# Performance work log

Hardware: AMD Instinct MI355X
Metric: run time of the kernel (lower is better)

The kernel has to match this reference:

```python
import jax, jax.numpy as jnp
import numpy as np

B, S, D = 2, 2048, 4096
H, G, HD = 32, 8, 128          # num_heads, num_kv_groups, head_dim
GROUP = H // G                  # group_size = 4
SCALE = HD ** -0.5


def setup_inputs() -> dict:
    key = jax.random.key(0)
    ks = jax.random.split(key, 6)
    x = jax.random.normal(ks[0], (B, S, D), dtype=jnp.float32)
    # Linear weights stored as [in, out] (y = x @ W), no bias, 0.02 init scale
    Wq = jax.random.normal(ks[1], (D, H * HD), dtype=jnp.float32) * 0.02
    Wk = jax.random.normal(ks[2], (D, G * HD), dtype=jnp.float32) * 0.02
    Wv = jax.random.normal(ks[3], (D, G * HD), dtype=jnp.float32) * 0.02
    Wo = jax.random.normal(ks[4], (H * HD, D), dtype=jnp.float32) * 0.02
    # RoPE tables: [S, HD], duplicated-half layout (rotate-half convention)
    inv_freq = 1.0 / (10000.0 ** (jnp.arange(0, HD, 2, dtype=jnp.float32) / HD))
    angles = jnp.arange(S, dtype=jnp.float32)[:, None] * inv_freq[None, :]  # [S, HD/2]
    angles = jnp.concatenate([angles, angles], axis=-1)                      # [S, HD]
    cos = jnp.cos(angles)
    sin = jnp.sin(angles)
    # causal mask: True = masked (strict upper triangle)
    mask = jnp.triu(jnp.ones((S, S), dtype=bool), k=1)
    return {"x": x, "Wq": Wq, "Wk": Wk, "Wv": Wv, "Wo": Wo,
            "cos": cos, "sin": sin, "mask": mask, "start_pos": 0}


def _rope(t, cos, sin, offset):
    # t: [B, h, S, HD]; cos/sin: [S_total, HD]
    n = t.shape[2]
    c = jax.lax.dynamic_slice_in_dim(cos, offset, n, axis=0)  # [n, HD]
    s = jax.lax.dynamic_slice_in_dim(sin, offset, n, axis=0)
    t1, t2 = t[..., : HD // 2], t[..., HD // 2:]
    rotated = jnp.concatenate([-t2, t1], axis=-1)
    return t * c[None, None] + rotated * s[None, None]


def reference(x, Wq, Wk, Wv, Wo, cos, sin, mask, start_pos):
    # projections
    q = (x @ Wq).reshape(B, S, H, HD).transpose(0, 2, 1, 3)   # [B,H,S,HD]
    k = (x @ Wk).reshape(B, S, G, HD).transpose(0, 2, 1, 3)   # [B,G,S,HD]
    v = (x @ Wv).reshape(B, S, G, HD).transpose(0, 2, 1, 3)   # [B,G,S,HD]
    # RoPE (no cache: prev_len = 0)
    q = _rope(q, cos, sin, start_pos) * SCALE
    k = _rope(k, cos, sin, start_pos)
    # GQA: expand kv groups to full heads (repeat_interleave along head dim)
    k_r = jnp.repeat(k, GROUP, axis=1)                         # [B,H,S,HD]
    v_r = jnp.repeat(v, GROUP, axis=1)
    scores = jnp.einsum('bhqd,bhkd->bhqk', q, k_r)             # [B,H,S,S]
    scores = jnp.where(mask[None, None], -jnp.inf, scores)
    w = jax.nn.softmax(scores, axis=-1)
    ctx = jnp.einsum('bhqk,bhkd->bhqd', w, v_r)                # [B,H,S,HD]
    ctx = ctx.transpose(0, 2, 1, 3).reshape(B, S, H * HD)
    out = ctx @ Wo                                             # [B,S,D]
    return out
```

## Files before the change

### kernel.cpp

```cpp
#include <hip/hip_runtime.h>
#include <hip/hip_bf16.h>
#include <math.h>

#define B_ 2
#define S_ 2048
#define D_ 4096
#define H_ 32
#define G_ 8
#define HD_ 128
#define GROUP_ 4
#define SCALE_ 0.08838834764831845f

typedef short bfv8 __attribute__((ext_vector_type(8)));
typedef float f32x4 __attribute__((ext_vector_type(4)));

__device__ __forceinline__ f32x4 mfma16(bfv8 a, bfv8 b, f32x4 c) {
  return __builtin_amdgcn_mfma_f32_16x16x32_bf16(a, b, c, 0, 0, 0);
}

__device__ __forceinline__ ushort f2bf_bits(float f) {
  __hip_bfloat16 h = __float2bfloat16(f);
  return *reinterpret_cast<ushort*>(&h);
}

__device__ __forceinline__ void gload16(const short* g, short* l) {
  __builtin_amdgcn_global_load_lds(
      (const __attribute__((address_space(1))) void*)g,
      (__attribute__((address_space(3))) void*)l, 16, 0, 0);
}

__global__ __launch_bounds__(256) void k_cvt(const float* __restrict__ in,
                                             ushort* __restrict__ out, int n4) {
  int i = blockIdx.x * 256 + threadIdx.x;
  if (i >= n4) return;
  float4 v = *(const float4*)(in + (size_t)i * 4);
  ushort4 o;
  o.x = f2bf_bits(v.x); o.y = f2bf_bits(v.y); o.z = f2bf_bits(v.z); o.w = f2bf_bits(v.w);
  *(ushort4*)(out + (size_t)i * 4) = o;
}

__global__ __launch_bounds__(256) void k_transpose(const float* __restrict__ in,
                                                   ushort* __restrict__ out,
                                                   int R, int C) {
  __shared__ ushort tile[32][33];
  int bc = blockIdx.x * 32;
  int br = blockIdx.y * 32;
  int tx = threadIdx.x;
  int ty = threadIdx.y;
  for (int ii = 0; ii < 4; ii++) {
    int i = ty + ii * 8;
    tile[i][tx] = f2bf_bits(in[(size_t)(br + i) * C + bc + tx]);
  }
  __syncthreads();
  for (int ii = 0; ii < 4; ii++) {
    int i = ty + ii * 8;
    out[(size_t)(bc + i) * R + br + tx] = tile[tx][i];
  }
}

__global__ __launch_bounds__(256) void k_transpose_v(const ushort* __restrict__ v,
                                                     ushort* __restrict__ vt) {
  __shared__ ushort tile[32][33];
  int bg = blockIdx.z;
  int b = bg / G_, g = bg % G_;
  int s0 = blockIdx.y * 32;
  int h0 = blockIdx.x * 32;
  int tx = threadIdx.x, ty = threadIdx.y;
  const ushort* src = v + (size_t)b * S_ * G_ * HD_ + (size_t)g * HD_;
  ushort* dst = vt + (size_t)(b * G_ + g) * HD_ * S_;
  for (int ii = 0; ii < 4; ii++) {
    int i = ty + ii * 8;
    tile[i][tx] = src[(size_t)(s0 + i) * (G_ * HD_) + h0 + tx];
  }
  __syncthreads();
  for (int ii = 0; ii < 4; ii++) {
    int i = ty + ii * 8;
    dst[(size_t)(h0 + i) * S_ + s0 + tx] = tile[tx][i];
  }
}

__global__ __launch_bounds__(64) void k_rope(__hip_bfloat16* __restrict__ t,
                                             const float* __restrict__ cosb,
                                             const float* __restrict__ sinb,
                                             int nheads, float scale) {
  int blk = blockIdx.x;
  int head = blk % nheads;
  int row = blk / nheads;
  int s = row & (S_ - 1);
  int l = threadIdx.x;
  size_t base = (size_t)row * nheads * HD_ + (size_t)head * HD_;
  float x1 = __bfloat162float(t[base + l]);
  float x2 = __bfloat162float(t[base + 64 + l]);
  float c1 = cosb[s * HD_ + l];
  float sn1 = sinb[s * HD_ + l];
  float c2 = cosb[s * HD_ + 64 + l];
  float sn2 = sinb[s * HD_ + 64 + l];
  t[base + l] = __float2bfloat16((x1 * c1 - x2 * sn1) * scale);
  t[base + 64 + l] = __float2bfloat16((x2 * c2 + x1 * sn2) * scale);
}

template <typename OT>
__global__ __launch_bounds__(256) void k_gemm_bt(const __hip_bfloat16* __restrict__ Ab,
                                                 const __hip_bfloat16* __restrict__ BTb,
                                                 OT* __restrict__ Cb,
                                                 int M, int N, int K) {
  __shared__ short sA[128 * 32];
  __shared__ short sB[128 * 32];
  int t = threadIdx.x;
  int w = t >> 6;
  int l = t & 63;
  int row0 = blockIdx.y * 128;
  int col0 = blockIdx.x * 128;
  int wr = (w >> 1) * 64;
  int wc = (w & 1) * 64;
  int fr = l & 15;
  int fq = l >> 4;
  int fo = fq * 8;
  int srow = l >> 2;
  int schk = (l & 3) * 8;

  const short* gA = (const short*)Ab;
  const short* gB = (const short*)BTb;

  f32x4 acc[4][4];
#pragma unroll
  for (int m = 0; m < 4; m++)
#pragma unroll
    for (int n = 0; n < 4; n++) acc[m][n] = (f32x4){0.f, 0.f, 0.f, 0.f};

  for (int k0 = 0; k0 < K; k0 += 32) {
    __syncthreads();
#pragma unroll
    for (int j = 0; j < 2; j++) {
      int r = w * 32 + j * 16;
      gload16(gA + (size_t)(row0 + r + srow) * K + k0 + schk, &sA[r * 32]);
      gload16(gB + (size_t)(col0 + r + srow) * K + k0 + schk, &sB[r * 32]);
    }
    __syncthreads();
    bfv8 af[4], bff[4];
#pragma unroll
    for (int m = 0; m < 4; m++) af[m] = *(const bfv8*)(sA + (wr + m * 16 + fr) * 32 + fo);
#pragma unroll
    for (int n = 0; n < 4; n++) bff[n] = *(const bfv8*)(sB + (wc + n * 16 + fr) * 32 + fo);
#pragma unroll
    for (int m = 0; m < 4; m++)
#pragma unroll
      for (int n = 0; n < 4; n++)
        acc[m][n] = mfma16(af[m], bff[n], acc[m][n]);
  }
#pragma unroll
  for (int m = 0; m < 4; m++)
#pragma unroll
    for (int n = 0; n < 4; n++)
#pragma unroll
      for (int j = 0; j < 4; j++) {
        int r = row0 + wr + m * 16 + fq * 4 + j;
        int c = col0 + wc + n * 16 + fr;
        if constexpr (__is_same(OT, float)) {
          Cb[(size_t)r * N + c] = acc[m][n][j];
        } else {
          Cb[(size_t)r * N + c] = __float2bfloat16(acc[m][n][j]);
        }
      }
}

template <typename OT>
__global__ __launch_bounds__(512, 2) void k_gemm256(const __hip_bfloat16* __restrict__ Ab,
                                                    const __hip_bfloat16* __restrict__ BTb,
                                                    OT* __restrict__ Cb,
                                                    int M, int N, int K) {
  __shared__ short sA[2][2][8192];
  __shared__ short sB[2][2][8192];
  int tid = threadIdx.x;
  int wid = tid >> 6;
  int l = tid & 63;
  int wr = (wid >> 2) * 128;
  int wc = (wid & 3) * 64;
  int fr = l & 15, fq = l >> 4;
  int cswz = (fq ^ ((fr >> 1) & 3)) * 8;
  int row0 = blockIdx.y * 256, col0 = blockIdx.x * 256;
  int sr = l >> 2;
  int schunk = ((l & 3) ^ (((wid * 16 + sr) >> 1) & 3)) * 8;
  const short* gA = (const short*)Ab;
  const short* gB = (const short*)BTb;

  f32x4 acc[8][4];
#pragma unroll
  for (int m = 0; m < 8; m++)
#pragma unroll
    for (int n = 0; n < 4; n++) acc[m][n] = (f32x4){0.f, 0.f, 0.f, 0.f};

#define STAGE256(buf, kh, isB, kt)                                                   \
  {                                                                                  \
    const short* g_ = (isB) ? gB : gA;                                               \
    int b0_ = (isB) ? col0 : row0;                                                   \
    short* s_ = (isB) ? &sB[buf][kh][0] : &sA[buf][kh][0];                           \
    int k0_ = (kt) * 64 + (kh) * 32;                                                 \
    _Pragma("unroll")                                                                \
    for (int i_ = 0; i_ < 2; i_++) {                                                 \
      int r_ = i_ * 128 + wid * 16 + sr;                                             \
      gload16(g_ + (size_t)(b0_ + r_) * K + k0_ + schunk,                            \
              s_ + (i_ * 128 + wid * 16) * 32);                                      \
    }                                                                                \
  }

  bfv8 bf[4];
#define COMPUTE256(cur, kh, mg, loadB)                                               \
  {                                                                                  \
    if (loadB) {                                                                     \
      _Pragma("unroll")                                                              \
      for (int n_ = 0; n_ < 4; n_++)                                                 \
        bf[n_] = *(const bfv8*)&sB[cur][kh][(wc + n_ * 16 + fr) * 32 + cswz];        \
    }                                                                                \
    bfv8 af_[4];                                                                     \
    _Pragma("unroll")                                                                \
    for (int j_ = 0; j_ < 4; j_++)                                                   \
      af_[j_] = *(const bfv8*)&sA[cur][kh][(wr + ((mg) * 4 + j_) * 16 + fr) * 32 + cswz]; \
    __builtin_amdgcn_s_setprio(1);                                                   \
    _Pragma("unroll")                                                                \
    for (int j_ = 0; j_ < 4; j_++)                                                   \
      _Pragma("unroll")                                                              \
      for (int n_ = 0; n_ < 4; n_++)                                                 \
        acc[(mg) * 4 + j_][n_] = mfma16(af_[j_], bf[n_], acc[(mg) * 4 + j_][n_]);    \
    __builtin_amdgcn_s_setprio(0);                                                   \
  }

  int NT = K / 64;
  STAGE256(0, 0, false, 0);
  STAGE256(0, 0, true, 0);
  STAGE256(0, 1, false, 0);
  STAGE256(0, 1, true, 0);

  for (int t = 0; t < NT - 1; t++) {
    int cur = t & 1, nxt = cur ^ 1;
    asm volatile("s_waitcnt vmcnt(4)" ::: "memory");
    __builtin_amdgcn_s_barrier();
    STAGE256(nxt, 0, false, t + 1);
    COMPUTE256(cur, 0, 0, true);
    STAGE256(nxt, 0, true, t + 1);
    COMPUTE256(cur, 0, 1, false);
    asm volatile("s_waitcnt vmcnt(4)" ::: "memory");
    __builtin_amdgcn_s_barrier();
    STAGE256(nxt, 1, false, t + 1);
    COMPUTE256(cur, 1, 0, true);
    STAGE256(nxt, 1, true, t + 1);
    COMPUTE256(cur, 1, 1, false);
  }
  {
    int cur = (NT - 1) & 1;
    asm volatile("s_waitcnt vmcnt(4)" ::: "memory");
    __builtin_amdgcn_s_barrier();
    COMPUTE256(cur, 0, 0, true);
    COMPUTE256(cur, 0, 1, false);
    asm volatile("s_waitcnt vmcnt(0)" ::: "memory");
    __builtin_amdgcn_s_barrier();
    COMPUTE256(cur, 1, 0, true);
    COMPUTE256(cur, 1, 1, false);
  }
#undef STAGE256
#undef COMPUTE256

#pragma unroll
  for (int m = 0; m < 8; m++)
#pragma unroll
    for (int n = 0; n < 4; n++)
#pragma unroll
      for (int j = 0; j < 4; j++) {
        int r = row0 + wr + m * 16 + fq * 4 + j;
        int c = col0 + wc + n * 16 + fr;
        if constexpr (__is_same(OT, float)) {
          Cb[(size_t)r * N + c] = acc[m][n][j];
        } else {
          Cb[(size_t)r * N + c] = __float2bfloat16(acc[m][n][j]);
        }
      }
}

#define PSTR 68
__global__ __launch_bounds__(512) void k_attn2(const __hip_bfloat16* __restrict__ Qb,
                                               const __hip_bfloat16* __restrict__ Kb,
                                               const __hip_bfloat16* __restrict__ VTb,
                                               __hip_bfloat16* __restrict__ ctx) {
  __shared__ short sK[64 * 128];
  __shared__ short sV[128 * 64];
  __shared__ short sP[8][16 * PSTR];

  const int nQB = S_ / 128;
  int blk = blockIdx.x;
  int qb = (nQB - 1) - (blk % nQB);
  int bh = blk / nQB;
  int h = bh % H_;
  int b = bh / H_;
  int g = h / GROUP_;
  int q0 = qb * 128;

  int t = threadIdx.x;
  int wid = t >> 6;
  int l = t & 63;
  int fr = l & 15, fq = l >> 4, fo = fq * 8;
  int wq0 = q0 + wid * 16;

  const short* qp = (const short*)Qb + (size_t)b * S_ * H_ * HD_ + (size_t)h * HD_;
  const short* kp = (const short*)Kb + (size_t)b * S_ * G_ * HD_ + (size_t)g * HD_;
  const short* vp = (const short*)VTb + (size_t)(b * G_ + g) * HD_ * S_;

  bfv8 qf[4];
#pragma unroll
  for (int c = 0; c < 4; c++)
    qf[c] = *(const bfv8*)(qp + (size_t)(wq0 + fr) * (H_ * HD_) + c * 32 + fo);

  f32x4 acc[8];
#pragma unroll
  for (int n = 0; n < 8; n++) acc[n] = (f32x4){0.f, 0.f, 0.f, 0.f};
  float m[4], ll[4];
#pragma unroll
  for (int j = 0; j < 4; j++) { m[j] = -INFINITY; ll[j] = 0.f; }

  int krow_i = l >> 4;
  int kchk = l & 15;
  int vrow_i = l >> 3;
  int vchk = l & 7;

  int nkt = 2 * qb + 2;
  for (int kt = 0; kt < nkt; kt++) {
    int k0 = kt * 64;
#pragma unroll
    for (int j = 0; j < 2; j++) {
      int base = wid * 8 + j * 4;
      int r = base + krow_i;
      gload16(kp + (size_t)(k0 + r) * (G_ * HD_) + ((kchk ^ (r & 7)) * 8), &sK[base * 128]);
    }
#pragma unroll
    for (int j = 0; j < 2; j++) {
      int base = wid * 16 + j * 8;
      int r = base + vrow_i;
      gload16(vp + (size_t)r * S_ + k0 + ((vchk ^ (r & 7)) * 8), &sV[base * 64]);
    }
    __syncthreads();

    f32x4 sf[4];
#pragma unroll
    for (int ks = 0; ks < 4; ks++) {
      sf[ks] = (f32x4){0.f, 0.f, 0.f, 0.f};
      int row = ks * 16 + fr;
      int rx = row & 7;
#pragma unroll
      for (int c = 0; c < 4; c++) {
        bfv8 kf = *(const bfv8*)&sK[row * 128 + (((c * 4 + fq) ^ rx) * 8)];
        sf[ks] = mfma16(qf[c], kf, sf[ks]);
      }
    }

    float p[4][4], sc[4], red[4];
#pragma unroll
    for (int j = 0; j < 4; j++) {
      int q = wq0 + fq * 4 + j;
#pragma unroll
      for (int ks = 0; ks < 4; ks++)
        if (k0 + ks * 16 + fr > q) sf[ks][j] = -INFINITY;
      red[j] = fmaxf(fmaxf(sf[0][j], sf[1][j]), fmaxf(sf[2][j], sf[3][j]));
    }
#pragma unroll
    for (int off = 1; off < 16; off <<= 1)
#pragma unroll
      for (int j = 0; j < 4; j++)
        red[j] = fmaxf(red[j], __shfl_xor(red[j], off, 64));
#pragma unroll
    for (int j = 0; j < 4; j++) {
      float nm = fmaxf(m[j], red[j]);
      sc[j] = __expf(m[j] - nm);
      m[j] = nm;
#pragma unroll
      for (int ks = 0; ks < 4; ks++) p[ks][j] = __expf(sf[ks][j] - nm);
      red[j] = (p[0][j] + p[1][j]) + (p[2][j] + p[3][j]);
    }
#pragma unroll
    for (int off = 1; off < 16; off <<= 1)
#pragma unroll
      for (int j = 0; j < 4; j++)
        red[j] += __shfl_xor(red[j], off, 64);
#pragma unroll
    for (int j = 0; j < 4; j++) {
      ll[j] = ll[j] * sc[j] + red[j];
#pragma unroll
      for (int n = 0; n < 8; n++) acc[n][j] *= sc[j];
#pragma unroll
      for (int ks = 0; ks < 4; ks++)
        sP[wid][(fq * 4 + j) * PSTR + ks * 16 + fr] = f2bf_bits(p[ks][j]);
    }

    bfv8 pa0 = *(const bfv8*)&sP[wid][fr * PSTR + fo];
    bfv8 pa1 = *(const bfv8*)&sP[wid][fr * PSTR + 32 + fo];
#pragma unroll
    for (int n = 0; n < 8; n++) {
      int row = n * 16 + fr;
      int rx = row & 7;
      bfv8 vf0 = *(const bfv8*)&sV[row * 64 + ((fq ^ rx) * 8)];
      bfv8 vf1 = *(const bfv8*)&sV[row * 64 + (((4 + fq) ^ rx) * 8)];
      acc[n] = mfma16(pa0, vf0, acc[n]);
      acc[n] = mfma16(pa1, vf1, acc[n]);
    }
    __syncthreads();
  }

#pragma unroll
  for (int n = 0; n < 8; n++)
#pragma unroll
    for (int j = 0; j < 4; j++) {
      int q = wq0 + fq * 4 + j;
      float o = acc[n][j] / ll[j];
      ctx[(size_t)(b * S_ + q) * (H_ * HD_) + h * HD_ + n * 16 + fr] = __float2bfloat16(o);
    }
}

extern "C" void kernel_launch(void* const* d_in, const int* in_sizes, int n_in,
                              void* d_out, int out_size, void* d_ws, size_t ws_size,
                              hipStream_t stream) {
  (void)in_sizes; (void)n_in; (void)out_size; (void)ws_size;
  const float* x    = (const float*)d_in[0];
  const float* Wq   = (const float*)d_in[1];
  const float* Wk   = (const float*)d_in[2];
  const float* Wv   = (const float*)d_in[3];
  const float* Wo   = (const float*)d_in[4];
  const float* cosb = (const float*)d_in[5];
  const float* sinb = (const float*)d_in[6];

  char* ws = (char*)d_ws;
  __hip_bfloat16* xb  = (__hip_bfloat16*)(ws + 0);
  __hip_bfloat16* WqT = (__hip_bfloat16*)(ws + 33554432);
  __hip_bfloat16* WkT = (__hip_bfloat16*)(ws + 67108864);
  __hip_bfloat16* WvT = (__hip_bfloat16*)(ws + 75497472);
  __hip_bfloat16* Qb  = (__hip_bfloat16*)(ws + 83886080);
  __hip_bfloat16* Kb  = (__hip_bfloat16*)(ws + 117440512);
  __hip_bfloat16* Vb  = (__hip_bfloat16*)(ws + 125829120);
  __hip_bfloat16* VTb = (__hip_bfloat16*)(ws + 134217728);
  __hip_bfloat16* Cx  = xb;

  dim3 tb(32, 8);
  k_cvt<<<(B_ * S_ * D_ / 4 + 255) / 256, 256, 0, stream>>>(x, (ushort*)xb, B_ * S_ * D_ / 4);
  k_transpose<<<dim3(128, 128), tb, 0, stream>>>(Wq, (ushort*)WqT, 4096, 4096);
  k_transpose<<<dim3(32, 128), tb, 0, stream>>>(Wk, (ushort*)WkT, 4096, 1024);
  k_transpose<<<dim3(32, 128), tb, 0, stream>>>(Wv, (ushort*)WvT, 4096, 1024);

  k_gemm256<__hip_bfloat16><<<dim3(16, 16), 512, 0, stream>>>(xb, WqT, Qb, 4096, 4096, 4096);
  k_gemm_bt<__hip_bfloat16><<<dim3(8, 32), 256, 0, stream>>>(xb, WkT, Kb, 4096, 1024, 4096);
  k_gemm_bt<__hip_bfloat16><<<dim3(8, 32), 256, 0, stream>>>(xb, WvT, Vb, 4096, 1024, 4096);

  k_transpose<<<dim3(128, 128), tb, 0, stream>>>(Wo, (ushort*)WqT, 4096, 4096);

  k_rope<<<4096 * 32, 64, 0, stream>>>(Qb, cosb, sinb, 32, SCALE_);
  k_rope<<<4096 * 8, 64, 0, stream>>>(Kb, cosb, sinb, 8, 1.0f);

  k_transpose_v<<<dim3(4, 64, 16), tb, 0, stream>>>((const ushort*)Vb, (ushort*)VTb);

  k_attn2<<<B_ * H_ * (S_ / 128), 512, 0, stream>>>(Qb, Kb, VTb, Cx);

  k_gemm256<float><<<dim3(16, 16), 512, 0, stream>>>(Cx, WqT, (float*)d_out, 4096, 4096, 4096);
}
```

Baseline: 829.5 us.

## Process two GQA heads per attention block to reuse staged K/V tiles

```diff
diff --git a/kernel.cpp b/kernel.cpp
--- a/kernel.cpp
+++ b/kernel.cpp
@@ -277,7 +277,7 @@
 }
 
 #define PSTR 68
-__global__ __launch_bounds__(512) void k_attn2(const __hip_bfloat16* __restrict__ Qb,
+__global__ __launch_bounds__(512) void k_attn4(const __hip_bfloat16* __restrict__ Qb,
                                                const __hip_bfloat16* __restrict__ Kb,
                                                const __hip_bfloat16* __restrict__ VTb,
                                                __hip_bfloat16* __restrict__ ctx) {
@@ -288,10 +288,12 @@
   const int nQB = S_ / 128;
   int blk = blockIdx.x;
   int qb = (nQB - 1) - (blk % nQB);
-  int bh = blk / nQB;
-  int h = bh % H_;
-  int b = bh / H_;
-  int g = h / GROUP_;
+  int rest = blk / nQB;
+  int pr = rest & 1;
+  int bg = rest >> 1;
+  int g = bg % G_;
+  int b = bg / G_;
+  int hA = g * GROUP_ + pr * 2;
   int q0 = qb * 128;
 
   int t = threadIdx.x;
@@ -300,26 +302,99 @@
   int fr = l & 15, fq = l >> 4, fo = fq * 8;
   int wq0 = q0 + wid * 16;
 
-  const short* qp = (const short*)Qb + (size_t)b * S_ * H_ * HD_ + (size_t)h * HD_;
+  const short* qpA = (const short*)Qb + (size_t)b * S_ * H_ * HD_ + (size_t)hA * HD_;
+  const short* qpB = qpA + HD_;
   const short* kp = (const short*)Kb + (size_t)b * S_ * G_ * HD_ + (size_t)g * HD_;
   const short* vp = (const short*)VTb + (size_t)(b * G_ + g) * HD_ * S_;
 
-  bfv8 qf[4];
-#pragma unroll
-  for (int c = 0; c < 4; c++)
-    qf[c] = *(const bfv8*)(qp + (size_t)(wq0 + fr) * (H_ * HD_) + c * 32 + fo);
-
-  f32x4 acc[8];
-#pragma unroll
-  for (int n = 0; n < 8; n++) acc[n] = (f32x4){0.f, 0.f, 0.f, 0.f};
-  float m[4], ll[4];
-#pragma unroll
-  for (int j = 0; j < 4; j++) { m[j] = -INFINITY; ll[j] = 0.f; }
+  bfv8 qfA[4], qfB[4];
+#pragma unroll
+  for (int c = 0; c < 4; c++) {
+    qfA[c] = *(const bfv8*)(qpA + (size_t)(wq0 + fr) * (H_ * HD_) + c * 32 + fo);
+    qfB[c] = *(const bfv8*)(qpB + (size_t)(wq0 + fr) * (H_ * HD_) + c * 32 + fo);
+  }
+
+  f32x4 accA[8], accB[8];
+#pragma unroll
+  for (int n = 0; n < 8; n++) {
+    accA[n] = (f32x4){0.f, 0.f, 0.f, 0.f};
+    accB[n] = (f32x4){0.f, 0.f, 0.f, 0.f};
+  }
+  float mA[4], llA[4], mB[4], llB[4];
+#pragma unroll
+  for (int j = 0; j < 4; j++) {
+    mA[j] = -INFINITY; llA[j] = 0.f;
+    mB[j] = -INFINITY; llB[j] = 0.f;
+  }
 
   int krow_i = l >> 4;
   int kchk = l & 15;
   int vrow_i = l >> 3;
   int vchk = l & 7;
+
+#define PROC_HEAD(QF, MM, LL, ACC)                                                   \
+  {                                                                                  \
+    f32x4 sf[4];                                                                     \
+    _Pragma("unroll")                                                                \
+    for (int ks = 0; ks < 4; ks++) {                                                 \
+      sf[ks] = (f32x4){0.f, 0.f, 0.f, 0.f};                                          \
+      int row = ks * 16 + fr;                                                        \
+      int rx = row & 7;                                                              \
+      _Pragma("unroll")                                                              \
+      for (int c = 0; c < 4; c++) {                                                  \
+        bfv8 kf = *(const bfv8*)&sK[row * 128 + (((c * 4 + fq) ^ rx) * 8)];          \
+        sf[ks] = mfma16(QF[c], kf, sf[ks]);                                          \
+      }                                                                              \
+    }                                                                                \
+    float p[4][4], sc[4], red[4];                                                    \
+    _Pragma("unroll")                                                                \
+    for (int j = 0; j < 4; j++) {                                                    \
+      int q = wq0 + fq * 4 + j;                                                      \
+      _Pragma("unroll")                                                              \
+      for (int ks = 0; ks < 4; ks++)                                                 \
+        if (k0 + ks * 16 + fr > q) sf[ks][j] = -INFINITY;                            \
+      red[j] = fmaxf(fmaxf(sf[0][j], sf[1][j]), fmaxf(sf[2][j], sf[3][j]));          \
+    }                                                                                \
+    _Pragma("unroll")                                                                \
+    for (int off = 1; off < 16; off <<= 1)                                           \
+      _Pragma("unroll")                                                              \
+      for (int j = 0; j < 4; j++)                                                    \
+        red[j] = fmaxf(red[j], __shfl_xor(red[j], off, 64));                         \
+    _Pragma("unroll")                                                                \
+    for (int j = 0; j < 4; j++) {                                                    \
+      float nm = fmaxf(MM[j], red[j]);                                               \
+      sc[j] = __expf(MM[j] - nm);                                                    \
+      MM[j] = nm;                                                                    \
+      _Pragma("unroll")                                                              \
+      for (int ks = 0; ks < 4; ks++) p[ks][j] = __expf(sf[ks][j] - nm);              \
+      red[j] = (p[0][j] + p[1][j]) + (p[2][j] + p[3][j]);                            \
+    }                                                                                \
+    _Pragma("unroll")                                                                \
+    for (int off = 1; off < 16; off <<= 1)                                           \
+      _Pragma("unroll")                                                              \
+      for (int j = 0; j < 4; j++)                                                    \
+        red[j] += __shfl_xor(red[j], off, 64);                                       \
+    _Pragma("unroll")                                                                \
+    for (int j = 0; j < 4; j++) {                                                    \
+      LL[j] = LL[j] * sc[j] + red[j];                                                \
+      _Pragma("unroll")                                                              \
+      for (int n = 0; n < 8; n++) ACC[n][j] *= sc[j];                                \
+      _Pragma("unroll")                                                              \
+      for (int ks = 0; ks < 4; ks++)                                                 \
+        sP[wid][(fq * 4 + j) * PSTR + ks * 16 + fr] = f2bf_bits(p[ks][j]);           \
+    }                                                                                \
+    bfv8 pa0 = *(const bfv8*)&sP[wid][fr * PSTR + fo];                               \
+    bfv8 pa1 = *(const bfv8*)&sP[wid][fr * PSTR + 32 + fo];                          \
+    _Pragma("unroll")                                                                \
+    for (int n = 0; n < 8; n++) {                                                    \
+      int row = n * 16 + fr;                                                         \
+      int rx = row & 7;                                                              \
+      bfv8 vf0 = *(const bfv8*)&sV[row * 64 + ((fq ^ rx) * 8)];                      \
+      bfv8 vf1 = *(const bfv8*)&sV[row * 64 + (((4 + fq) ^ rx) * 8)];                \
+      ACC[n] = mfma16(pa0, vf0, ACC[n]);                                             \
+      ACC[n] = mfma16(pa1, vf1, ACC[n]);                                             \
+    }                                                                                \
+  }
 
   int nkt = 2 * qb + 2;
   for (int kt = 0; kt < nkt; kt++) {
@@ -338,78 +413,21 @@
     }
     __syncthreads();
 
-    f32x4 sf[4];
-#pragma unroll
-    for (int ks = 0; ks < 4; ks++) {
-      sf[ks] = (f32x4){0.f, 0.f, 0.f, 0.f};
-      int row = ks * 16 + fr;
-      int rx = row & 7;
-#pragma unroll
-      for (int c = 0; c < 4; c++) {
-        bfv8 kf = *(const bfv8*)&sK[row * 128 + (((c * 4 + fq) ^ rx) * 8)];
-        sf[ks] = mfma16(qf[c], kf, sf[ks]);
-      }
-    }
-
-    float p[4][4], sc[4], red[4];
+    PROC_HEAD(qfA, mA, llA, accA);
+    PROC_HEAD(qfB, mB, llB, accB);
+
+    __syncthreads();
+  }
+#undef PROC_HEAD
+
+#pragma unroll
+  for (int n = 0; n < 8; n++)
 #pragma unroll
     for (int j = 0; j < 4; j++) {
       int q = wq0 + fq * 4 + j;
-#pragma unroll
-      for (int ks = 0; ks < 4; ks++)
-        if (k0 + ks * 16 + fr > q) sf[ks][j] = -INFINITY;
-      red[j] = fmaxf(fmaxf(sf[0][j], sf[1][j]), fmaxf(sf[2][j], sf[3][j]));
-    }
-#pragma unroll
-    for (int off = 1; off < 16; off <<= 1)
-#pragma unroll
-      for (int j = 0; j < 4; j++)
-        red[j] = fmaxf(red[j], __shfl_xor(red[j], off, 64));
-#pragma unroll
-    for (int j = 0; j < 4; j++) {
-      float nm = fmaxf(m[j], red[j]);
-      sc[j] = __expf(m[j] - nm);
-      m[j] = nm;
-#pragma unroll
-      for (int ks = 0; ks < 4; ks++) p[ks][j] = __expf(sf[ks][j] - nm);
-      red[j] = (p[0][j] + p[1][j]) + (p[2][j] + p[3][j]);
-    }
-#pragma unroll
-    for (int off = 1; off < 16; off <<= 1)
-#pragma unroll
-      for (int j = 0; j < 4; j++)
-        red[j] += __shfl_xor(red[j], off, 64);
-#pragma unroll
-    for (int j = 0; j < 4; j++) {
-      ll[j] = ll[j] * sc[j] + red[j];
-#pragma unroll
-      for (int n = 0; n < 8; n++) acc[n][j] *= sc[j];
-#pragma unroll
-      for (int ks = 0; ks < 4; ks++)
-        sP[wid][(fq * 4 + j) * PSTR + ks * 16 + fr] = f2bf_bits(p[ks][j]);
-    }
-
-    bfv8 pa0 = *(const bfv8*)&sP[wid][fr * PSTR + fo];
-    bfv8 pa1 = *(const bfv8*)&sP[wid][fr * PSTR + 32 + fo];
-#pragma unroll
-    for (int n = 0; n < 8; n++) {
-      int row = n * 16 + fr;
-      int rx = row & 7;
-      bfv8 vf0 = *(const bfv8*)&sV[row * 64 + ((fq ^ rx) * 8)];
-      bfv8 vf1 = *(const bfv8*)&sV[row * 64 + (((4 + fq) ^ rx) * 8)];
-      acc[n] = mfma16(pa0, vf0, acc[n]);
-      acc[n] = mfma16(pa1, vf1, acc[n]);
-    }
-    __syncthreads();
-  }
-
-#pragma unroll
-  for (int n = 0; n < 8; n++)
-#pragma unroll
-    for (int j = 0; j < 4; j++) {
-      int q = wq0 + fq * 4 + j;
-      float o = acc[n][j] / ll[j];
-      ctx[(size_t)(b * S_ + q) * (H_ * HD_) + h * HD_ + n * 16 + fr] = __float2bfloat16(o);
+      size_t rowbase = (size_t)(b * S_ + q) * (H_ * HD_);
+      ctx[rowbase + hA * HD_ + n * 16 + fr] = __float2bfloat16(accA[n][j] / llA[j]);
+      ctx[rowbase + (hA + 1) * HD_ + n * 16 + fr] = __float2bfloat16(accB[n][j] / llB[j]);
     }
 }
 
@@ -453,7 +471,7 @@
 
   k_transpose_v<<<dim3(4, 64, 16), tb, 0, stream>>>((const ushort*)Vb, (ushort*)VTb);
 
-  k_attn2<<<B_ * H_ * (S_ / 128), 512, 0, stream>>>(Qb, Kb, VTb, Cx);
+  k_attn4<<<B_ * G_ * 2 * (S_ / 128), 512, 0, stream>>>(Qb, Kb, VTb, Cx);
 
   k_gemm256<float><<<dim3(16, 16), 512, 0, stream>>>(Cx, WqT, (float*)d_out, 4096, 4096, 4096);
 }
```

Result: slower. 872.5 us (+5.2%).
